# Kernel tuning notes

Measured on AMD Instinct MI355X. Metric: run time of the kernel, lower is better.

The kernel has to match this reference:

```python
import jax, jax.numpy as jnp
import numpy as np
import math

B, T, D_MODEL, N_HEADS = 4, 2048, 1024, 16
D_HEAD = D_MODEL // N_HEADS


def _rope_freqs(t, d_head):
    inv = 1.0 / (10000.0 ** (np.arange(0, d_head, 2, dtype=np.float32) / d_head))
    ang = np.arange(t, dtype=np.float32)[:, None] * inv[None, :]  # (T, d_head//2)
    return jnp.asarray(np.cos(ang)), jnp.asarray(np.sin(ang))


def setup_inputs() -> dict:
    key = jax.random.key(0)
    k1, k2, k3, k4, k5 = jax.random.split(key, 5)
    s = 1.0 / math.sqrt(D_MODEL)
    x = jax.random.normal(k1, (B, T, D_MODEL), dtype=jnp.float32)
    mask = jnp.triu(jnp.ones((T, T), dtype=bool), k=1)  # causal: mask future positions
    freqs_cos, freqs_sin = _rope_freqs(T, D_HEAD)
    qkv_w = jax.random.uniform(k2, (3 * D_MODEL, D_MODEL), jnp.float32, -s, s)
    qkv_b = jax.random.uniform(k3, (3 * D_MODEL,), jnp.float32, -s, s)
    proj_w = jax.random.uniform(k4, (D_MODEL, D_MODEL), jnp.float32, -s, s)
    proj_b = jax.random.uniform(k5, (D_MODEL,), jnp.float32, -s, s)
    return {"x": x, "mask": mask, "freqs_cos": freqs_cos, "freqs_sin": freqs_sin,
            "qkv_w": qkv_w, "qkv_b": qkv_b, "proj_w": proj_w, "proj_b": proj_b}


def _apply_rope(t, cos, sin):
    # t: (B, H, T, D_HEAD); cos/sin: (T, D_HEAD//2), broadcast over B, H
    tp = t.reshape(*t.shape[:-1], -1, 2)
    a, b = tp[..., 0], tp[..., 1]
    out_r = a * cos - b * sin
    out_i = a * sin + b * cos
    return jnp.stack([out_r, out_i], axis=-1).reshape(t.shape)


def reference(x, mask, freqs_cos, freqs_sin, qkv_w, qkv_b, proj_w, proj_b):
    Bx, Tx, C = x.shape
    qkv = x @ qkv_w.T + qkv_b  # (B, T, 3C)
    q, k, v = jnp.split(qkv, 3, axis=-1)
    def heads(z):
        return z.reshape(Bx, Tx, N_HEADS, D_HEAD).transpose(0, 2, 1, 3)  # (B,H,T,dh)
    q, k, v = heads(q), heads(k), heads(v)
    q = _apply_rope(q, freqs_cos, freqs_sin)
    k = _apply_rope(k, freqs_cos, freqs_sin)
    att = jnp.einsum('bhqd,bhkd->bhqk', q, k) / math.sqrt(D_HEAD)
    att = jnp.where(mask, -jnp.inf, att)
    att = jax.nn.softmax(att, axis=-1)
    out = jnp.einsum('bhqk,bhkd->bhqd', att, v)
    out = out.transpose(0, 2, 1, 3).reshape(Bx, Tx, C)
    return out @ proj_w.T + proj_b
```

## Files before the change

kernel.cpp:

```cpp
#include <hip/hip_runtime.h>
#include <stdint.h>

#define BB 4
#define TT 2048
#define CC 1024
#define HH 16
#define DH 64
#define NQKV 3072

typedef __bf16 bf16_t;
typedef __attribute__((ext_vector_type(8))) __bf16 bf16x8;
typedef __attribute__((ext_vector_type(4))) float f32x4;

#define MFMA16(a, b, c) __builtin_amdgcn_mfma_f32_16x16x32_bf16((a), (b), (c), 0, 0, 0)

__device__ __forceinline__ void gll16(const void* g, void* l) {
  typedef const __attribute__((address_space(1))) void* gp_t;
  typedef __attribute__((address_space(3))) void* lp_t;
  __builtin_amdgcn_global_load_lds((gp_t)(uintptr_t)g, (lp_t)(uintptr_t)l, 16, 0, 0);
}

__global__ __launch_bounds__(256) void cvt_k(const float* __restrict__ src,
                                             bf16_t* __restrict__ dst, int n) {
  const int i8 = (blockIdx.x * 256 + threadIdx.x) * 8;
  if (i8 < n) {
    const f32x4 a = *(const f32x4*)(src + i8);
    const f32x4 b = *(const f32x4*)(src + i8 + 4);
    bf16x8 r;
    r[0] = (bf16_t)a[0]; r[1] = (bf16_t)a[1]; r[2] = (bf16_t)a[2]; r[3] = (bf16_t)a[3];
    r[4] = (bf16_t)b[0]; r[5] = (bf16_t)b[1]; r[6] = (bf16_t)b[2]; r[7] = (bf16_t)b[3];
    *(bf16x8*)(dst + i8) = r;
  }
}

template <int EPI>
__global__ __launch_bounds__(256) void gemm_k(
    const bf16_t* __restrict__ A, const bf16_t* __restrict__ W,
    const float* __restrict__ bias,
    const float* __restrict__ fcos, const float* __restrict__ fsin,
    void* __restrict__ out0v, bf16_t* __restrict__ out1,
    bf16_t* __restrict__ out2) {
  __shared__ bf16_t Alds[2][128 * 32];
  __shared__ bf16_t Blds[2][128 * 32];
  const int K = 1024;
  const int tid = threadIdx.x;
  const int lane = tid & 63, wave = tid >> 6;
  const int quad = lane >> 4, c = lane & 15;
  const int wm = wave >> 1, wn = wave & 1;

  const int nwgx = gridDim.x;
  const int d = blockIdx.y * nwgx + blockIdx.x;
  const int cpx = (nwgx * gridDim.y) >> 3;
  const int lg = (d & 7) * cpx + (d >> 3);
  const int bx = lg % nwgx, by = lg / nwgx;
  const int mbase = by * 128, nbase = bx * 128;

  f32x4 acc[4][4];
#pragma unroll
  for (int i = 0; i < 4; ++i)
#pragma unroll
    for (int j = 0; j < 4; ++j) acc[i][j] = (f32x4){0.f, 0.f, 0.f, 0.f};

  const int s0 = tid, s1 = tid + 256;
  const int r0 = s0 >> 2, cc0 = (s0 & 3) ^ (r0 & 3);
  const int r1 = s1 >> 2, cc1 = (s1 & 3) ^ (r1 & 3);
  const bf16_t* ag0 = A + (mbase + r0) * K + cc0 * 8;
  const bf16_t* ag1 = A + (mbase + r1) * K + cc1 * 8;
  const bf16_t* bg0 = W + (nbase + r0) * K + cc0 * 8;
  const bf16_t* bg1 = W + (nbase + r1) * K + cc1 * 8;

#define GSTAGE(BUF, KO)                        \
  {                                            \
    gll16(ag0 + (KO), &Alds[BUF][s0 * 8]);     \
    gll16(ag1 + (KO), &Alds[BUF][s1 * 8]);     \
    gll16(bg0 + (KO), &Blds[BUF][s0 * 8]);     \
    gll16(bg1 + (KO), &Blds[BUF][s1 * 8]);     \
  }

#define GSTEP(KS, CUR, STG)                                                    \
  {                                                                            \
    if (STG) GSTAGE((CUR) ^ 1, ((KS) + 1) * 32);                               \
    bf16x8 af[4], bfr[4];                                                      \
    _Pragma("unroll") for (int mi = 0; mi < 4; ++mi) {                         \
      const int row = wm * 64 + mi * 16 + c;                                   \
      af[mi] = *(const bf16x8*)&Alds[CUR][(row * 4 + (quad ^ (row & 3))) * 8]; \
    }                                                                          \
    _Pragma("unroll") for (int ni = 0; ni < 4; ++ni) {                         \
      const int row = wn * 64 + ni * 16 + c;                                   \
      bfr[ni] =                                                                \
          *(const bf16x8*)&Blds[CUR][(row * 4 + (quad ^ (row & 3))) * 8];      \
    }                                                                          \
    _Pragma("unroll") for (int mi = 0; mi < 4; ++mi)                           \
        _Pragma("unroll") for (int ni = 0; ni < 4; ++ni)                       \
            acc[mi][ni] = MFMA16(af[mi], bfr[ni], acc[mi][ni]);                \
    if (STG) {                                                                 \
      asm volatile("s_waitcnt vmcnt(0)" ::: "memory");                         \
      __builtin_amdgcn_s_barrier();                                            \
      asm volatile("" ::: "memory");                                           \
    }                                                                          \
  }

  GSTAGE(0, 0);
  asm volatile("s_waitcnt vmcnt(0)" ::: "memory");
  __builtin_amdgcn_s_barrier();
  asm volatile("" ::: "memory");

  for (int fj = 0; fj < 15; ++fj) {
    GSTEP(2 * fj, 0, 1)
    GSTEP(2 * fj + 1, 1, 1)
  }
  GSTEP(30, 0, 1)
  GSTEP(31, 1, 0)
#undef GSTEP
#undef GSTAGE

  const float qscale = 0.18033688011112042f;
#pragma unroll
  for (int mi = 0; mi < 4; ++mi) {
#pragma unroll
    for (int ni = 0; ni < 4; ++ni) {
      const int n = nbase + wn * 64 + ni * 16 + c;
      const float bv = bias[n];
#pragma unroll
      for (int r = 0; r < 4; ++r) {
        const int m = mbase + wm * 64 + mi * 16 + quad * 4 + r;
        float v = acc[mi][ni][r] + bv;
        if (EPI == 0) {
          bf16_t* out0 = (bf16_t*)out0v;
          const int sel = n >> 10;
          const int nl = n & 1023;
          const int h = nl >> 6, dd = nl & 63;
          const int b = m >> 11, t = m & 2047;
          const int dst = ((b * HH + h) * TT + t) * DH + dd;
          if (sel < 2) {
            const float pv = __shfl_xor(v, 1, 64);
            const int d2 = dd >> 1;
            const float cs = fcos[t * 32 + d2];
            const float sn = fsin[t * 32 + d2];
            float o = ((dd & 1) == 0) ? (v * cs - pv * sn) : (pv * sn + v * cs);
            if (sel == 0) {
              o *= qscale;
              out0[dst] = (bf16_t)o;
            } else {
              out1[dst] = (bf16_t)o;
            }
          } else {
            out2[dst] = (bf16_t)v;
          }
        } else {
          float* outf = (float*)out0v;
          outf[m * CC + n] = v;
        }
      }
    }
  }
}

__global__ __launch_bounds__(256, 4) void attn_k(const bf16_t* __restrict__ Q,
                                                 const bf16_t* __restrict__ Kv,
                                                 const bf16_t* __restrict__ V,
                                                 bf16_t* __restrict__ O) {
  __shared__ bf16_t KS[2][64 * 64];
  __shared__ bf16_t VtS[2][64 * 64];
  __shared__ bf16_t PS[4][16 * 64];

  const int tid = threadIdx.x;
  const int lane = tid & 63, wave = tid >> 6;
  const int quad = lane >> 4, c = lane & 15;
  const int d0 = blockIdx.x;
  const int bi = (d0 & 7) * 128 + (d0 >> 3);
  const int pair = bi & 15, h = (bi >> 4) & 15, b = bi >> 8;
  const int qtA = pair, qtB = 31 - pair;
  const int nA = qtA + 1;

  const bf16_t* Qh = Q + ((b * HH + h) * TT) * DH;
  const bf16_t* Kh = Kv + ((b * HH + h) * TT) * DH;
  const bf16_t* Vh = V + ((b * HH + h) * TT) * DH;

  const f32x4 zero4 = {0.f, 0.f, 0.f, 0.f};
  bf16x8 ones8;
#pragma unroll
  for (int i = 0; i < 8; ++i) ones8[i] = (bf16_t)1.0f;

  const int krow0 = tid >> 3, kc8 = tid & 7, krow1 = krow0 + 32;
  const bf16_t* kbase0 = Kh + krow0 * DH + kc8 * 8;
  const bf16_t* kbase1 = Kh + krow1 * DH + kc8 * 8;
  const int vsb = tid >> 2, vjp = tid & 3;
  const int vrg = vsb & 7, vc8 = vsb >> 3;
  const int vd0 = vc8 * 8 + vjp * 2, vd1 = vd0 + 1;
  const bf16_t* vbase = Vh + vrg * 8 * DH + vd0;

  const int sw = c & 7;
  const int e0 = c * 64 + (quad ^ sw) * 8;
  const int e1 = c * 64 + ((quad + 4) ^ sw) * 8;

  bf16x8 kr0, kr1;
  uint32_t vr[8];
  auto load_tile = [&](int eoff) {
    kr0 = *(const bf16x8*)(kbase0 + eoff);
    kr1 = *(const bf16x8*)(kbase1 + eoff);
    const bf16_t* vp = vbase + eoff;
#pragma unroll
    for (int i = 0; i < 8; ++i) vr[i] = *(const uint32_t*)(vp + i * DH);
  };
  auto store_tile = [&](int buf) {
    *(bf16x8*)&KS[buf][(krow0 * 8 + (kc8 ^ (krow0 & 7))) * 8] = kr0;
    *(bf16x8*)&KS[buf][(krow1 * 8 + (kc8 ^ (krow1 & 7))) * 8] = kr1;
    union { bf16x8 v; uint16_t u[8]; } colA, colB;
#pragma unroll
    for (int i = 0; i < 8; ++i) {
      colA.u[i] = (uint16_t)(vr[i] & 0xffffu);
      colB.u[i] = (uint16_t)(vr[i] >> 16);
    }
    *(bf16x8*)&VtS[buf][(vd0 * 8 + (vrg ^ (vd0 & 7))) * 8] = colA.v;
    *(bf16x8*)&VtS[buf][(vd1 * 8 + (vrg ^ (vd1 & 7))) * 8] = colB.v;
  };

  int qtbase = qtA * 64;
  bf16x8 qf0 = *(const bf16x8*)(Qh + (qtbase + wave * 16 + c) * DH + quad * 8);
  bf16x8 qf1 = *(const bf16x8*)(Qh + (qtbase + wave * 16 + c) * DH + 32 + quad * 8);

  f32x4 o_acc[4] = {zero4, zero4, zero4, zero4};
  float m_r[4] = {-1e30f, -1e30f, -1e30f, -1e30f};
  float l_r[4] = {0.f, 0.f, 0.f, 0.f};

  auto write_O = [&](int qtb) {
#pragma unroll
    for (int r = 0; r < 4; ++r) {
      const int qg = qtb + wave * 16 + quad * 4 + r;
      const float inv = 1.0f / l_r[r];
#pragma unroll
      for (int ni = 0; ni < 4; ++ni)
        O[(b * TT + qg) * CC + h * 64 + ni * 16 + c] =
            (bf16_t)(o_acc[ni][r] * inv);
    }
  };

  load_tile(0);
  store_tile(0);
  __syncthreads();
  int coff = 0;
  int kkey = 0;

#define ATTN_ITER(FI, CUR)                                                     \
  {                                                                            \
    const int fi_ = (FI);                                                      \
    const bool pre_ = fi_ < 32;                                                \
    const int noff_ = (fi_ + 1 == nA) ? 0 : coff + 64 * DH;                    \
    if (pre_) load_tile(noff_);                                                \
    bf16x8 kf0[4], kf1[4];                                                     \
    _Pragma("unroll") for (int ni = 0; ni < 4; ++ni) {                         \
      kf0[ni] = *(const bf16x8*)&KS[CUR][ni * 1024 + e0];                      \
      kf1[ni] = *(const bf16x8*)&KS[CUR][ni * 1024 + e1];                      \
    }                                                                          \
    f32x4 s[4];                                                                \
    _Pragma("unroll") for (int ni = 0; ni < 4; ++ni) {                         \
      f32x4 t = MFMA16(qf0, kf0[ni], zero4);                                   \
      t = MFMA16(qf1, kf1[ni], t);                                             \
      s[ni] = t;                                                               \
    }                                                                          \
    const int minq_ = qtbase + wave * 16;                                      \
    if (kkey + 63 > minq_) {                                                   \
      _Pragma("unroll") for (int ni = 0; ni < 4; ++ni)                         \
          _Pragma("unroll") for (int r = 0; r < 4; ++r) {                      \
        const int key_ = kkey + ni * 16 + c;                                   \
        const int qg_ = minq_ + quad * 4 + r;                                  \
        if (key_ > qg_) s[ni][r] = -1e30f;                                     \
      }                                                                        \
    }                                                                          \
                 \
    float mx_[4];                                                              \
    bool need_ = false;                                                        \
    _Pragma("unroll") for (int r = 0; r < 4; ++r) {                            \
      float mx = fmaxf(fmaxf(s[0][r], s[1][r]), fmaxf(s[2][r], s[3][r]));      \
      mx = fmaxf(mx, __shfl_xor(mx, 1, 64));                                   \
      mx = fmaxf(mx, __shfl_xor(mx, 2, 64));                                   \
      mx = fmaxf(mx, __shfl_xor(mx, 4, 64));                                   \
      mx = fmaxf(mx, __shfl_xor(mx, 8, 64));                                   \
      mx_[r] = mx;                                                             \
      need_ = need_ || (mx > m_r[r] + 8.0f);                                   \
    }                                                                          \
    if (__any(need_)) {                                                        \
      _Pragma("unroll") for (int r = 0; r < 4; ++r) {                          \
        const float mnew = fmaxf(m_r[r], mx_[r]);                              \
        const float al = __builtin_amdgcn_exp2f(m_r[r] - mnew);                \
        m_r[r] = mnew;                                                         \
        l_r[r] *= al;                                                          \
        _Pragma("unroll") for (int ni = 0; ni < 4; ++ni)                       \
            o_acc[ni][r] *= al;                                                \
      }                                                                        \
    }                                                                          \
    _Pragma("unroll") for (int ni = 0; ni < 4; ++ni)                           \
        _Pragma("unroll") for (int r = 0; r < 4; ++r) {                        \
      const float p = __builtin_amdgcn_exp2f(s[ni][r] - m_r[r]);               \
      const int prow_ = quad * 4 + r, pcol_ = ni * 16 + c;                     \
      PS[wave][(prow_ * 8 + ((pcol_ >> 3) ^ (prow_ & 7))) * 8 + (pcol_ & 7)] = \
          (bf16_t)p;                                                           \
    }                                                                          \
    asm volatile("s_waitcnt lgkmcnt(0)" ::: "memory");                         \
    const bf16x8 p0 = *(const bf16x8*)&PS[wave][e0];                           \
    const bf16x8 p1 = *(const bf16x8*)&PS[wave][e1];                           \
    f32x4 rs = MFMA16(p0, ones8, zero4);                                       \
    rs = MFMA16(p1, ones8, rs);                                                \
    _Pragma("unroll") for (int ni = 0; ni < 4; ++ni) {                         \
      const bf16x8 v0 = *(const bf16x8*)&VtS[CUR][ni * 1024 + e0];             \
      const bf16x8 v1 = *(const bf16x8*)&VtS[CUR][ni * 1024 + e1];             \
      o_acc[ni] = MFMA16(p0, v0, o_acc[ni]);                                   \
      o_acc[ni] = MFMA16(p1, v1, o_acc[ni]);                                   \
    }                                                                          \
    _Pragma("unroll") for (int r = 0; r < 4; ++r) l_r[r] += rs[r];             \
    if (fi_ == nA - 1) {                                                       \
      write_O(qtbase);                                                         \
      qtbase = qtB * 64;                                                       \
      qf0 = *(const bf16x8*)(Qh + (qtbase + wave * 16 + c) * DH + quad * 8);   \
      qf1 = *(const bf16x8*)(Qh + (qtbase + wave * 16 + c) * DH + 32 +         \
                             quad * 8);                                        \
      _Pragma("unroll") for (int r = 0; r < 4; ++r) {                          \
        m_r[r] = -1e30f;                                                       \
        l_r[r] = 0.f;                                                          \
      }                                                                        \
      _Pragma("unroll") for (int ni = 0; ni < 4; ++ni) o_acc[ni] = zero4;      \
    }                                                                          \
    if (pre_) store_tile(1 - (CUR));                                           \
    __syncthreads();                                                           \
    coff = noff_;                                                              \
    kkey = (fi_ + 1 == nA) ? 0 : kkey + 64;                                    \
  }

  for (int fj = 0; fj < 16; ++fj) {
    ATTN_ITER(2 * fj, 0)
    ATTN_ITER(2 * fj + 1, 1)
  }
  ATTN_ITER(32, 0)
#undef ATTN_ITER

  write_O(qtbase);
}

extern "C" void kernel_launch(void* const* d_in, const int* in_sizes, int n_in,
                              void* d_out, int out_size, void* d_ws,
                              size_t ws_size, hipStream_t stream) {
  const float *x = nullptr, *fcos = nullptr, *fsin = nullptr;
  const float *qkv_w = nullptr, *qkv_b = nullptr, *proj_w = nullptr, *proj_b = nullptr;
  for (int i = 0; i < n_in; ++i) {
    const int s = in_sizes[i];
    const float* p = (const float*)d_in[i];
    if (s == BB * TT * CC) x = p;
    else if (s == TT * (DH / 2)) { if (!fcos) fcos = p; else fsin = p; }
    else if (s == NQKV * CC) qkv_w = p;
    else if (s == NQKV) qkv_b = p;
    else if (s == CC * CC) proj_w = p;
    else if (s == CC) proj_b = p;
  }

  const size_t NE = (size_t)BB * TT * CC;
  bf16_t* Qb = (bf16_t*)d_ws;
  bf16_t* Kb = Qb + NE;
  bf16_t* Vb = Kb + NE;
  bf16_t* Ob = Vb + NE;
  bf16_t* xb = Ob;
  bf16_t* wqkvb = (bf16_t*)d_out;
  bf16_t* wpb = Qb;

  cvt_k<<<dim3((int)(NE / 2048)), 256, 0, stream>>>(x, xb, (int)NE);
  cvt_k<<<dim3(NQKV * CC / 2048), 256, 0, stream>>>(qkv_w, wqkvb, NQKV * CC);

  gemm_k<0><<<dim3(NQKV / 128, (BB * TT) / 128), 256, 0, stream>>>(
      xb, wqkvb, qkv_b, fcos, fsin, (void*)Qb, Kb, Vb);
  attn_k<<<dim3(BB * HH * 16), 256, 0, stream>>>(Qb, Kb, Vb, Ob);
  cvt_k<<<dim3(CC * CC / 2048), 256, 0, stream>>>(proj_w, wpb, CC * CC);
  gemm_k<1><<<dim3(CC / 128, (BB * TT) / 128), 256, 0, stream>>>(
      Ob, wpb, proj_b, nullptr, nullptr, d_out, nullptr, nullptr);
}
```

Baseline: 308.5 us.

## Compute transposed S tile so softmax row-max needs fewer shuffles and packed P stores

Swaps the MFMA operands so the score tile is transposed: each lane holds one query's scores across four keys per subtile. Row max now reduces in-lane over 16 values plus two cross-lane shuffles instead of four shuffles per row times four rows. Running max becomes one scalar per lane, and the rescale factor is broadcast back to the O layout by a shuffle. P is written to LDS as packed bf16x4 instead of scalar stores. It depends on the swizzle variable `sw` and `lane` being defined elsewhere, and the mask and LDS index mapping must match the transposed layout.

```diff
diff --git a/kernel.cpp b/kernel.cpp
--- a/kernel.cpp
+++ b/kernel.cpp
@@ -10,6 +10,7 @@
 
 typedef __bf16 bf16_t;
 typedef __attribute__((ext_vector_type(8))) __bf16 bf16x8;
+typedef __attribute__((ext_vector_type(4))) __bf16 bf16x4;
 typedef __attribute__((ext_vector_type(4))) float f32x4;
 
 #define MFMA16(a, b, c) __builtin_amdgcn_mfma_f32_16x16x32_bf16((a), (b), (c), 0, 0, 0)
@@ -221,7 +222,7 @@
   bf16x8 qf1 = *(const bf16x8*)(Qh + (qtbase + wave * 16 + c) * DH + 32 + quad * 8);
 
   f32x4 o_acc[4] = {zero4, zero4, zero4, zero4};
-  float m_r[4] = {-1e30f, -1e30f, -1e30f, -1e30f};
+  float m_s = -1e30f;
   float l_r[4] = {0.f, 0.f, 0.f, 0.f};
 
   auto write_O = [&](int qtb) {
@@ -253,49 +254,49 @@
       kf0[ni] = *(const bf16x8*)&KS[CUR][ni * 1024 + e0];                      \
       kf1[ni] = *(const bf16x8*)&KS[CUR][ni * 1024 + e1];                      \
     }                                                                          \
+    \
     f32x4 s[4];                                                                \
     _Pragma("unroll") for (int ni = 0; ni < 4; ++ni) {                         \
-      f32x4 t = MFMA16(qf0, kf0[ni], zero4);                                   \
-      t = MFMA16(qf1, kf1[ni], t);                                             \
+      f32x4 t = MFMA16(kf0[ni], qf0, zero4);                                   \
+      t = MFMA16(kf1[ni], qf1, t);                                             \
       s[ni] = t;                                                               \
     }                                                                          \
     const int minq_ = qtbase + wave * 16;                                      \
     if (kkey + 63 > minq_) {                                                   \
+      const int qg_ = minq_ + c;                                               \
       _Pragma("unroll") for (int ni = 0; ni < 4; ++ni)                         \
           _Pragma("unroll") for (int r = 0; r < 4; ++r) {                      \
-        const int key_ = kkey + ni * 16 + c;                                   \
-        const int qg_ = minq_ + quad * 4 + r;                                  \
+        const int key_ = kkey + ni * 16 + quad * 4 + r;                        \
         if (key_ > qg_) s[ni][r] = -1e30f;                                     \
       }                                                                        \
     }                                                                          \
+                      \
+    float a0_ = fmaxf(fmaxf(s[0][0], s[0][1]), fmaxf(s[0][2], s[0][3]));       \
+    float a1_ = fmaxf(fmaxf(s[1][0], s[1][1]), fmaxf(s[1][2], s[1][3]));       \
+    float a2_ = fmaxf(fmaxf(s[2][0], s[2][1]), fmaxf(s[2][2], s[2][3]));       \
+    float a3_ = fmaxf(fmaxf(s[3][0], s[3][1]), fmaxf(s[3][2], s[3][3]));       \
+    float mx = fmaxf(fmaxf(a0_, a1_), fmaxf(a2_, a3_));                        \
+    mx = fmaxf(mx, __shfl_xor(mx, 16, 64));                                    \
+    mx = fmaxf(mx, __shfl_xor(mx, 32, 64));                                    \
                  \
-    float mx_[4];                                                              \
-    bool need_ = false;                                                        \
-    _Pragma("unroll") for (int r = 0; r < 4; ++r) {                            \
-      float mx = fmaxf(fmaxf(s[0][r], s[1][r]), fmaxf(s[2][r], s[3][r]));      \
-      mx = fmaxf(mx, __shfl_xor(mx, 1, 64));                                   \
-      mx = fmaxf(mx, __shfl_xor(mx, 2, 64));                                   \
-      mx = fmaxf(mx, __shfl_xor(mx, 4, 64));                                   \
-      mx = fmaxf(mx, __shfl_xor(mx, 8, 64));                                   \
-      mx_[r] = mx;                                                             \
-      need_ = need_ || (mx > m_r[r] + 8.0f);                                   \
-    }                                                                          \
-    if (__any(need_)) {                                                        \
+    if (__any(mx > m_s + 8.0f)) {                                              \
+      const float mnew = fmaxf(m_s, mx);                                       \
+      const float al = __builtin_amdgcn_exp2f(m_s - mnew);                     \
+      m_s = mnew;                                                              \
       _Pragma("unroll") for (int r = 0; r < 4; ++r) {                          \
-        const float mnew = fmaxf(m_r[r], mx_[r]);                              \
-        const float al = __builtin_amdgcn_exp2f(m_r[r] - mnew);                \
-        m_r[r] = mnew;                                                         \
-        l_r[r] *= al;                                                          \
+        const float alD = __shfl(al, (lane & 48) | (quad * 4 + r), 64);        \
+        l_r[r] *= alD;                                                         \
         _Pragma("unroll") for (int ni = 0; ni < 4; ++ni)                       \
-            o_acc[ni][r] *= al;                                                \
+            o_acc[ni][r] *= alD;                                               \
       }                                                                        \
     }                                                                          \
-    _Pragma("unroll") for (int ni = 0; ni < 4; ++ni)                           \
-        _Pragma("unroll") for (int r = 0; r < 4; ++r) {                        \
-      const float p = __builtin_amdgcn_exp2f(s[ni][r] - m_r[r]);               \
-      const int prow_ = quad * 4 + r, pcol_ = ni * 16 + c;                     \
-      PS[wave][(prow_ * 8 + ((pcol_ >> 3) ^ (prow_ & 7))) * 8 + (pcol_ & 7)] = \
-          (bf16_t)p;                                                           \
+         \
+    _Pragma("unroll") for (int ni = 0; ni < 4; ++ni) {                         \
+      bf16x4 pk_;                                                              \
+      _Pragma("unroll") for (int r = 0; r < 4; ++r)                            \
+          pk_[r] = (bf16_t)__builtin_amdgcn_exp2f(s[ni][r] - m_s);             \
+      *(bf16x4*)&PS[wave][(c * 8 + ((2 * ni + (quad >> 1)) ^ sw)) * 8 +        \
+                          (quad & 1) * 4] = pk_;                               \
     }                                                                          \
     asm volatile("s_waitcnt lgkmcnt(0)" ::: "memory");                         \
     const bf16x8 p0 = *(const bf16x8*)&PS[wave][e0];                           \
@@ -315,10 +316,8 @@
       qf0 = *(const bf16x8*)(Qh + (qtbase + wave * 16 + c) * DH + quad * 8);   \
       qf1 = *(const bf16x8*)(Qh + (qtbase + wave * 16 + c) * DH + 32 +         \
                              quad * 8);                                        \
-      _Pragma("unroll") for (int r = 0; r < 4; ++r) {                          \
-        m_r[r] = -1e30f;                                                       \
-        l_r[r] = 0.f;                                                          \
-      }                                                                        \
+      m_s = -1e30f;                                                            \
+      _Pragma("unroll") for (int r = 0; r < 4; ++r) l_r[r] = 0.f;              \
       _Pragma("unroll") for (int ni = 0; ni < 4; ++ni) o_acc[ni] = zero4;      \
     }                                                                          \
     if (pre_) store_tile(1 - (CUR));                                           \
```

After: 284.4 us. -7.8%, faster.
